# Performance work log

Hardware: AMD Instinct MI355X
Metric: run time of the kernel (lower is better)

The kernel has to match this reference:

```python
import jax, jax.numpy as jnp
import numpy as np

N_NODES = 100000
N_EDGES = 1200000
IN_FEATS = 128
HIDDEN = 64
OUT_FEATS = 40


def setup_inputs() -> dict:
    key = jax.random.key(0)
    k1, k2, k3, k4, k5 = jax.random.split(key, 5)
    x = jax.random.normal(k1, (N_NODES, IN_FEATS), dtype=jnp.float32)
    edge_index = jax.random.randint(k2, (2, N_EDGES), 0, N_NODES, dtype=jnp.int64)
    W1 = jax.random.normal(k3, (IN_FEATS, HIDDEN), dtype=jnp.float32) * (1.0 / np.sqrt(IN_FEATS))
    b1 = jnp.zeros((HIDDEN,), dtype=jnp.float32)
    W2 = jax.random.normal(k4, (HIDDEN, HIDDEN), dtype=jnp.float32) * (1.0 / np.sqrt(HIDDEN))
    b2 = jnp.zeros((HIDDEN,), dtype=jnp.float32)
    Wc = jax.random.normal(k5, (HIDDEN, OUT_FEATS), dtype=jnp.float32) * (1.0 / np.sqrt(HIDDEN))
    bc = jnp.zeros((OUT_FEATS,), dtype=jnp.float32)
    return {"x": x, "edge_index": edge_index, "W1": W1, "b1": b1,
            "W2": W2, "b2": b2, "Wc": Wc, "bc": bc}


def _gcn_norm(edge_index, n_nodes):
    # add self-loops, then symmetric normalization deg^{-1/2}[src] * deg^{-1/2}[dst]
    loops = jnp.arange(n_nodes, dtype=edge_index.dtype)
    src = jnp.concatenate([edge_index[0], loops])
    dst = jnp.concatenate([edge_index[1], loops])
    ones = jnp.ones(src.shape[0], dtype=jnp.float32)
    deg = jax.ops.segment_sum(ones, dst, num_segments=n_nodes)  # in-degree incl. self-loop
    dinv = jnp.where(deg > 0, jax.lax.rsqrt(deg), 0.0)
    norm = dinv[src] * dinv[dst]  # [E+N]
    return src, dst, norm


def _gcn_conv(h, W, b, src, dst, norm, n_nodes):
    h = h @ W                          # [N, F_out] dense transform first (PyG GCNConv)
    msg = h[src] * norm[:, None]       # gather + normalize, [E+N, F_out]
    out = jax.ops.segment_sum(msg, dst, num_segments=n_nodes)  # scatter-add
    return out + b


def reference(x, edge_index, W1, b1, W2, b2, Wc, bc):
    n = x.shape[0]
    src, dst, norm = _gcn_norm(edge_index, n)
    # dropout is identity in eval mode
    h = jax.nn.relu(_gcn_conv(x, W1, b1, src, dst, norm, n))
    embedding = _gcn_conv(h, W2, b2, src, dst, norm, n)
    logits = embedding @ Wc + bc
    soft_label = jax.nn.softmax(logits, axis=1)
    hard_label = jnp.argmax(soft_label, axis=1)
    return (logits, embedding, soft_label, hard_label)
```

## Files before the change

### kernel.cpp

```cpp
#include <hip/hip_runtime.h>
#include <hip/hip_bf16.h>
#include <math.h>

typedef __hip_bfloat16 bf16;
typedef __attribute__((ext_vector_type(8))) short bf16x8;
typedef __attribute__((ext_vector_type(4))) float f32x4;

__device__ __forceinline__ float loadf(const void* p, size_t i, bool f32m) {
    return f32m ? ((const float*)p)[i]
                : __bfloat162float(((const bf16*)p)[i]);
}
__device__ __forceinline__ void storef(void* p, size_t i, float v, bool f32m) {
    if (f32m) ((float*)p)[i] = v;
    else      ((bf16*)p)[i] = __float2bfloat16(v);
}
__device__ __forceinline__ int ldidx(const int* w, size_t e, bool e64, size_t E, int row) {
    return e64 ? w[2 * (row * E + e)] : w[row * E + e];
}

__device__ __forceinline__ unsigned short f2bf(float f) {
    unsigned u = __float_as_uint(f);
    unsigned r = (u + 0x7FFFu + ((u >> 16) & 1u)) >> 16;
    return (unsigned short)r;
}
__device__ __forceinline__ float bf2f(unsigned short h) {
    return __uint_as_float(((unsigned)h) << 16);
}

__global__ void k_detect(const void* x, const int* ei, float* flags) {
    int lane = threadIdx.x;
    const unsigned short* hx = (const unsigned short*)x;
    unsigned short u = hx[2 * lane];
    int ex = (u >> 7) & 0xFF;
    bool tame = (ex >= 117 && ex <= 136);
    unsigned long long mt = __ballot(tame);
    unsigned long long mz = __ballot(ei[2 * lane + 1] != 0);
    if (lane == 0) {
        flags[0] = (__popcll(mt) >= 48) ? 0.0f : 1.0f;
        flags[1] = (mz == 0ULL) ? 1.0f : 0.0f;
    }
}


__global__ void k_zero_small(int* __restrict__ p, int m) {
    int i = blockIdx.x * 256 + threadIdx.x;
    if (i < m) p[i] = 0;
}

#define SCB_EPT 16

__global__ __launch_bounds__(256) void k_bucket_hist(const int* __restrict__ ei,
                                                     const float* __restrict__ flags,
                                                     int* __restrict__ bcnt, int E, int NB) {
    __shared__ int lcnt[512];
    bool e64 = flags[1] > 0.5f;
    int tid = threadIdx.x;
    for (int i = tid; i < NB; i += 256) lcnt[i] = 0;
    __syncthreads();
    int base = blockIdx.x * 256 * SCB_EPT;
#pragma unroll
    for (int j = 0; j < SCB_EPT; ++j) {
        int e = base + j * 256 + tid;
        if (e < E) atomicAdd(&lcnt[ldidx(ei, e, e64, E, 1) >> 8], 1);
    }
    __syncthreads();
    for (int i = tid; i < NB; i += 256) {
        int c = lcnt[i];
        if (c) atomicAdd(&bcnt[i], c);
    }
}

__global__ __launch_bounds__(512) void k_scan_buckets(const int* __restrict__ bcnt,
                                                      int* __restrict__ bbase,
                                                      int* __restrict__ bcur, int NB) {
    __shared__ int sh[512];
    int tid = threadIdx.x;
    int v = (tid < NB) ? bcnt[tid] : 0;
    sh[tid] = v;
    __syncthreads();
    for (int off = 1; off < 512; off <<= 1) {
        int t = (tid >= off) ? sh[tid - off] : 0;
        __syncthreads();
        sh[tid] += t;
        __syncthreads();
    }
    if (tid < NB) {
        int ex = sh[tid] - v;
        bbase[tid] = ex;
        bcur[tid] = ex;
    }
    if (tid == 0) bbase[NB] = sh[511];
}

__global__ __launch_bounds__(256) void k_bucket_scatter(const int* __restrict__ ei,
                                                        const float* __restrict__ flags,
                                                        int* __restrict__ bcur,
                                                        int2* __restrict__ recs,
                                                        int E, int NB) {
    __shared__ int lcnt[512], lrank[512], lbase[512];
    bool e64 = flags[1] > 0.5f;
    int tid = threadIdx.x;
    for (int i = tid; i < NB; i += 256) { lcnt[i] = 0; lrank[i] = 0; }
    __syncthreads();
    int base = blockIdx.x * 256 * SCB_EPT;
    int s[SCB_EPT], d[SCB_EPT];
#pragma unroll
    for (int j = 0; j < SCB_EPT; ++j) {
        int e = base + j * 256 + tid;
        if (e < E) {
            s[j] = ldidx(ei, e, e64, E, 0);
            d[j] = ldidx(ei, e, e64, E, 1);
            atomicAdd(&lcnt[d[j] >> 8], 1);
        } else d[j] = -1;
    }
    __syncthreads();
    for (int i = tid; i < NB; i += 256) {
        int c = lcnt[i];
        lbase[i] = c ? atomicAdd(&bcur[i], c) : 0;
    }
    __syncthreads();
#pragma unroll
    for (int j = 0; j < SCB_EPT; ++j) {
        if (d[j] >= 0) {
            int b = d[j] >> 8;
            int r = atomicAdd(&lrank[b], 1);
            recs[lbase[b] + r] = make_int2(s[j], d[j]);
        }
    }
}

__global__ __launch_bounds__(256) void k_bucket_csr(const int2* __restrict__ recs,
                                                    const int* __restrict__ bbase,
                                                    int* __restrict__ rowptr,
                                                    float* __restrict__ dinv,
                                                    int* __restrict__ srcs,
                                                    int n, int E) {
    __shared__ int lcnt[256];
    __shared__ int lcur[256];
    int b = blockIdx.x, tid = threadIdx.x;
    int e0 = bbase[b], e1 = bbase[b + 1];
    lcnt[tid] = 0;
    __syncthreads();
    for (int i = e0 + tid; i < e1; i += 256)
        atomicAdd(&lcnt[recs[i].y & 255], 1);
    __syncthreads();
    int c = lcnt[tid];
    lcur[tid] = c;
    __syncthreads();
    for (int off = 1; off < 256; off <<= 1) {
        int t = (tid >= off) ? lcur[tid - off] : 0;
        __syncthreads();
        lcur[tid] += t;
        __syncthreads();
    }
    int rp = bbase[b] + lcur[tid] - c;
    int node = (b << 8) + tid;
    if (node < n) {
        rowptr[node] = rp;
        dinv[node] = rsqrtf((float)(c + 1));
    }
    lcur[tid] = rp;
    __syncthreads();
    for (int i = e0 + tid; i < e1; i += 256) {
        int2 r = recs[i];
        int pos = atomicAdd(&lcur[r.y & 255], 1);
        srcs[pos] = r.x;
    }
    if (b == 0 && tid == 0) rowptr[n] = E;
}

template <int K, bool XALWAYSF32>
__global__ __launch_bounds__(256) void k_gconv_mfma(const void* __restrict__ Xa,
                                                    const void* __restrict__ Xb,
                                                    const void* __restrict__ W,
                                                    const float* __restrict__ flags,
                                                    const float* __restrict__ rowscale,
                                                    float* __restrict__ out, int n) {
    constexpr int KP = K + 8;
    __shared__ __align__(16) unsigned short wh[64 * KP];
    __shared__ __align__(16) unsigned short wlo[64 * KP];
    bool f32m = flags[0] > 0.5f;
    const void* X = f32m ? Xa : Xb;
    bool xf32 = XALWAYSF32 || f32m;
    int tid = threadIdx.x;

    if (f32m) {
        for (int i = tid * 4; i < K * 64; i += 1024) {
            int k = i >> 6, c = i & 63;
            float4 v = *(const float4*)((const float*)W + i);
            float vv[4] = {v.x, v.y, v.z, v.w};
#pragma unroll
            for (int q = 0; q < 4; ++q) {
                unsigned short h = f2bf(vv[q]);
                unsigned short l = f2bf(vv[q] - bf2f(h));
                wh [(c + q) * KP + k] = h;
                wlo[(c + q) * KP + k] = l;
            }
        }
    } else {
        for (int i = tid; i < K * 64; i += 256) {
            int k = i >> 6, c = i & 63;
            wh [c * KP + k] = ((const unsigned short*)W)[i];
            wlo[c * KP + k] = 0;
        }
    }
    __syncthreads();

    int lane = tid & 63, wv = tid >> 6;
    int r0 = blockIdx.x * 64 + wv * 16;
    int mrow = lane & 15, kgrp = lane >> 4;
    int row = r0 + mrow;
    bool rok = (row < n);

    f32x4 acc[4];
#pragma unroll
    for (int ct = 0; ct < 4; ++ct) acc[ct] = (f32x4){0.0f, 0.0f, 0.0f, 0.0f};

    const float*          xrf = (const float*)X          + (size_t)(rok ? row : 0) * K;
    const unsigned short* xrb = (const unsigned short*)X + (size_t)(rok ? row : 0) * K;

#pragma unroll
    for (int ks = 0; ks < K / 32; ++ks) {
        int kb = ks * 32 + kgrp * 8;
        bf16x8 ahi = {0, 0, 0, 0, 0, 0, 0, 0};
        bf16x8 alo = {0, 0, 0, 0, 0, 0, 0, 0};
        if (rok) {
            if (xf32) {
                float4 v0 = *(const float4*)(xrf + kb);
                float4 v1 = *(const float4*)(xrf + kb + 4);
                float fv[8] = {v0.x, v0.y, v0.z, v0.w, v1.x, v1.y, v1.z, v1.w};
#pragma unroll
                for (int j = 0; j < 8; ++j) {
                    unsigned short h = f2bf(fv[j]);
                    ahi[j] = (short)h;
                    alo[j] = (short)f2bf(fv[j] - bf2f(h));
                }
            } else {
                ahi = *(const bf16x8*)(xrb + kb);
            }
        }
#pragma unroll
        for (int ct = 0; ct < 4; ++ct) {
            int c = ct * 16 + mrow;
            bf16x8 bhi = *(const bf16x8*)&wh [c * KP + kb];
            bf16x8 blo = *(const bf16x8*)&wlo[c * KP + kb];
            acc[ct] = __builtin_amdgcn_mfma_f32_16x16x32_bf16(ahi, bhi, acc[ct], 0, 0, 0);
            acc[ct] = __builtin_amdgcn_mfma_f32_16x16x32_bf16(ahi, blo, acc[ct], 0, 0, 0);
            acc[ct] = __builtin_amdgcn_mfma_f32_16x16x32_bf16(alo, bhi, acc[ct], 0, 0, 0);
        }
    }

    float sc[4];
    int obase = r0 + kgrp * 4;
#pragma unroll
    for (int r = 0; r < 4; ++r)
        sc[r] = (obase + r < n) ? rowscale[obase + r] : 0.0f;
#pragma unroll
    for (int ct = 0; ct < 4; ++ct) {
#pragma unroll
        for (int r = 0; r < 4; ++r) {
            int orow = obase + r;
            if (orow < n)
                out[(size_t)orow * 64 + ct * 16 + mrow] = acc[ct][r] * sc[r];
        }
    }
}

template <int EP>
__global__ __launch_bounds__(256) void k_agg(const float* __restrict__ t,
                                             const float* __restrict__ dinv,
                                             const int* __restrict__ rowptr,
                                             const int* __restrict__ srcs,
                                             const void* __restrict__ bias,
                                             const float* __restrict__ flags,
                                             void* __restrict__ d_out, size_t emb_base,
                                             float* __restrict__ B_ws, int n) {
    bool f32m = flags[0] > 0.5f;
    int wvid = (blockIdx.x * 256 + threadIdx.x) >> 6;
    int lane = threadIdx.x & 63;
    int grp = lane >> 4;
    int sub = lane & 15;
    int v = wvid * 4 + grp;
    if (v >= n) return;

    float dv = dinv[v];
    int e0 = rowptr[v], e1 = rowptr[v + 1];
    int deg = e1 - e0;

    float4 acc = *(const float4*)(t + ((size_t)v << 6) + sub * 4);

    for (int base = 0; base < deg; base += 16) {
        int idx = base + sub;
        int sid = (idx < deg) ? srcs[e0 + idx] : -1;
        int cnt = deg - base; if (cnt > 16) cnt = 16;
        for (int j = 0; j < cnt; j += 4) {
            int gb = grp * 16 + j;
            int s0 = __shfl(sid, gb + 0, 64);
            int s1 = __shfl(sid, gb + 1, 64);
            int s2 = __shfl(sid, gb + 2, 64);
            int s3 = __shfl(sid, gb + 3, 64);
            float4 r0 = {0, 0, 0, 0}, r1 = {0, 0, 0, 0}, r2 = {0, 0, 0, 0}, r3 = {0, 0, 0, 0};
            if (s0 >= 0) r0 = *(const float4*)(t + ((size_t)s0 << 6) + sub * 4);
            if (s1 >= 0) r1 = *(const float4*)(t + ((size_t)s1 << 6) + sub * 4);
            if (s2 >= 0) r2 = *(const float4*)(t + ((size_t)s2 << 6) + sub * 4);
            if (s3 >= 0) r3 = *(const float4*)(t + ((size_t)s3 << 6) + sub * 4);
            acc.x += (r0.x + r1.x) + (r2.x + r3.x);
            acc.y += (r0.y + r1.y) + (r2.y + r3.y);
            acc.z += (r0.z + r1.z) + (r2.z + r3.z);
            acc.w += (r0.w + r1.w) + (r2.w + r3.w);
        }
    }

    float4 bias4;
    if (f32m) {
        bias4 = ((const float4*)bias)[sub];
    } else {
        const bf16* bp = (const bf16*)bias + sub * 4;
        bias4.x = __bfloat162float(bp[0]); bias4.y = __bfloat162float(bp[1]);
        bias4.z = __bfloat162float(bp[2]); bias4.w = __bfloat162float(bp[3]);
    }

    float4 o;
    o.x = acc.x * dv + bias4.x;
    o.y = acc.y * dv + bias4.y;
    o.z = acc.z * dv + bias4.z;
    o.w = acc.w * dv + bias4.w;
    if (EP == 0) {
        o.x = fmaxf(o.x, 0.0f); o.y = fmaxf(o.y, 0.0f);
        o.z = fmaxf(o.z, 0.0f); o.w = fmaxf(o.w, 0.0f);
    }
    size_t ob = ((size_t)v << 6) + sub * 4;
    if (f32m) {
        *(float4*)((float*)d_out + emb_base + ob) = o;
    } else {
        *(float4*)&B_ws[ob] = o;
        if (EP == 1) {
            __hip_bfloat162 h0, h1;
            h0.x = __float2bfloat16(o.x); h0.y = __float2bfloat16(o.y);
            h1.x = __float2bfloat16(o.z); h1.y = __float2bfloat16(o.w);
            __hip_bfloat162* p = (__hip_bfloat162*)((bf16*)d_out + emb_base + ob);
            p[0] = h0; p[1] = h1;
        }
    }
}


__device__ __forceinline__ void store_row40(void* out, size_t base, const float* a, bool f32m) {
    if (f32m) {
        float4* p = (float4*)((float*)out + base);
#pragma unroll
        for (int q = 0; q < 10; ++q) {
            float4 st = {a[q * 4 + 0], a[q * 4 + 1], a[q * 4 + 2], a[q * 4 + 3]};
            p[q] = st;
        }
    } else {
        __hip_bfloat162* p = (__hip_bfloat162*)((bf16*)out + base);
#pragma unroll
        for (int i = 0; i < 20; ++i) {
            __hip_bfloat162 h;
            h.x = __float2bfloat16(a[2 * i]);
            h.y = __float2bfloat16(a[2 * i + 1]);
            p[i] = h;
        }
    }
}

__global__ __launch_bounds__(256) void k_classifier(const float* __restrict__ flags,
                                                    const void* __restrict__ Wc,
                                                    const void* __restrict__ bc,
                                                    void* __restrict__ out,
                                                    size_t emb_base, size_t soft_base,
                                                    size_t hard_base,
                                                    const float* __restrict__ B_ws,
                                                    int n) {
    __shared__ __align__(16) float wcs[64 * 40];
    __shared__ __align__(16) float bcs[40];
    bool f32m = flags[0] > 0.5f;
    const float* emb = f32m ? ((const float*)out + emb_base) : B_ws;
    int tid = threadIdx.x;

    if (f32m) {
        for (int i = tid * 4; i < 64 * 40; i += 1024)
            *(float4*)&wcs[i] = *(const float4*)((const float*)Wc + i);
    } else {
        for (int i = tid; i < 64 * 40; i += 256)
            wcs[i] = __bfloat162float(((const bf16*)Wc)[i]);
    }
    if (tid < 40) bcs[tid] = loadf(bc, tid, f32m);
    __syncthreads();

    int node = blockIdx.x * 256 + tid;
    if (node >= n) return;

    float acc[40];
#pragma unroll
    for (int q = 0; q < 10; ++q) {
        float4 b4 = *(const float4*)&bcs[q * 4];
        acc[q * 4 + 0] = b4.x; acc[q * 4 + 1] = b4.y;
        acc[q * 4 + 2] = b4.z; acc[q * 4 + 3] = b4.w;
    }

    const float4* erow = (const float4*)(emb + (size_t)node * 64);
#pragma unroll 2
    for (int j = 0; j < 16; ++j) {
        float4 e4 = erow[j];
        float ev[4] = {e4.x, e4.y, e4.z, e4.w};
#pragma unroll
        for (int kk = 0; kk < 4; ++kk) {
            float e = ev[kk];
            const float4* wr = (const float4*)&wcs[(j * 4 + kk) * 40];
#pragma unroll
            for (int q = 0; q < 10; ++q) {
                float4 w = wr[q];
                acc[q * 4 + 0] = fmaf(e, w.x, acc[q * 4 + 0]);
                acc[q * 4 + 1] = fmaf(e, w.y, acc[q * 4 + 1]);
                acc[q * 4 + 2] = fmaf(e, w.z, acc[q * 4 + 2]);
                acc[q * 4 + 3] = fmaf(e, w.w, acc[q * 4 + 3]);
            }
        }
    }

    store_row40(out, (size_t)node * 40, acc, f32m);

    float m0 = acc[0], m1 = acc[1], m2 = acc[2], m3 = acc[3];
#pragma unroll
    for (int q = 1; q < 10; ++q) {
        m0 = fmaxf(m0, acc[q * 4 + 0]); m1 = fmaxf(m1, acc[q * 4 + 1]);
        m2 = fmaxf(m2, acc[q * 4 + 2]); m3 = fmaxf(m3, acc[q * 4 + 3]);
    }
    float m = fmaxf(fmaxf(m0, m1), fmaxf(m2, m3));

    int bi = 63;
#pragma unroll
    for (int c = 0; c < 40; ++c)
        if (acc[c] == m && c < bi) bi = c;

    float s = 0.0f;
#pragma unroll
    for (int c = 0; c < 40; ++c) {
        float e = expf(acc[c] - m);
        acc[c] = e;
        s += e;
    }
    float rs = 1.0f / s;
#pragma unroll
    for (int c = 0; c < 40; ++c) acc[c] *= rs;

    store_row40(out, soft_base + (size_t)node * 40, acc, f32m);
    storef(out, hard_base + node, (float)bi, f32m);
}

extern "C" void kernel_launch(void* const* d_in, const int* in_sizes, int n_in,
                              void* d_out, int out_size, void* d_ws, size_t ws_size,
                              hipStream_t stream) {
    const void* x  = d_in[0];
    const int*  ei = (const int*)d_in[1];
    const void* W1 = d_in[2];
    const void* b1 = d_in[3];
    const void* W2 = d_in[4];
    const void* b2 = d_in[5];
    const void* Wc = d_in[6];
    const void* bc = d_in[7];

    const int n = in_sizes[0] / 128;
    const int E = in_sizes[1] / 2;
    const int NB = (n + 255) / 256;

    float* ws    = (float*)d_ws;
    const size_t npad = (((size_t)n + 1023) / 1024) * 1024;
    const size_t Epad = (((size_t)E + 255) / 256) * 256;
    float* flags  = ws;
    int*   bcnt   = (int*)(ws + 256);
    int*   bbase  = (int*)(ws + 768);
    int*   bcur   = (int*)(ws + 1536);
    int*   rowptr = (int*)(ws + 2048);
    float* dinv   = (float*)(rowptr + npad);
    int*   srcs   = (int*)(dinv + npad);
    float* A      = (float*)(srcs + Epad);
    float* B_ws   = A + (size_t)n * 64;
    int2*  recs   = (int2*)B_ws;

    const size_t emb_base  = (size_t)n * 40;
    const size_t soft_base = (size_t)n * 104;
    const size_t hard_base = (size_t)n * 144;
    float* h1_f32m = (float*)d_out + emb_base;

    const int gS  = (E + 256 * SCB_EPT - 1) / (256 * SCB_EPT);
    const int gG  = (n + 63) / 64;
    const int gW  = (n + 15) / 16;
    const int gC  = (n + 255) / 256;

    k_detect<<<1, 64, 0, stream>>>(x, ei, flags);

    k_zero_small<<<2, 256, 0, stream>>>(bcnt, 512);
    k_bucket_hist<<<gS, 256, 0, stream>>>(ei, flags, bcnt, E, NB);
    k_scan_buckets<<<1, 512, 0, stream>>>(bcnt, bbase, bcur, NB);
    k_bucket_scatter<<<gS, 256, 0, stream>>>(ei, flags, bcur, recs, E, NB);
    k_bucket_csr<<<NB, 256, 0, stream>>>(recs, bbase, rowptr, dinv, srcs, n, E);

    k_gconv_mfma<128, false><<<gG, 256, 0, stream>>>(x, x, W1, flags, dinv, A, n);
    k_agg<0><<<gW, 256, 0, stream>>>(A, dinv, rowptr, srcs, b1, flags,
                                     d_out, emb_base, B_ws, n);

    k_gconv_mfma<64, true><<<gG, 256, 0, stream>>>(h1_f32m, B_ws, W2, flags, dinv, A, n);
    k_agg<1><<<gW, 256, 0, stream>>>(A, dinv, rowptr, srcs, b2, flags,
                                     d_out, emb_base, B_ws, n);

    k_classifier<<<gC, 256, 0, stream>>>(flags, Wc, bc, d_out,
                                         emb_base, soft_base, hard_base, B_ws, n);
}
```

Before: 314.6 us.

## Replace two-level bucket sort CSR build with per-node degree count and atomic fill

Replaces the bucket histogram, scatter and per-bucket local sort with a direct pipeline. Global atomics count per-node in-degree, a three-stage prefix scan produces rowptr and dinv, and a fill kernel places each source with a per-node atomic cursor. This removes the intermediate int2 record buffer and its extra pass. In exchange it uses many contended global atomics and issues two extra small launches, and the neighbour order within each row becomes nondeterministic.

```diff
diff --git a/kernel.cpp b/kernel.cpp
--- a/kernel.cpp
+++ b/kernel.cpp
@@ -42,40 +42,50 @@
 }
 
 
-__global__ void k_zero_small(int* __restrict__ p, int m) {
+#define SCB_EPT 16
+
+__global__ void k_zero_deg(int* __restrict__ deg, int n) {
     int i = blockIdx.x * 256 + threadIdx.x;
-    if (i < m) p[i] = 0;
-}
-
-#define SCB_EPT 16
-
-__global__ __launch_bounds__(256) void k_bucket_hist(const int* __restrict__ ei,
-                                                     const float* __restrict__ flags,
-                                                     int* __restrict__ bcnt, int E, int NB) {
-    __shared__ int lcnt[512];
+    if (i < n) deg[i] = 0;
+}
+
+__global__ __launch_bounds__(256) void k_deg(const int* __restrict__ ei,
+                                             const float* __restrict__ flags,
+                                             int* __restrict__ deg, int E) {
     bool e64 = flags[1] > 0.5f;
     int tid = threadIdx.x;
-    for (int i = tid; i < NB; i += 256) lcnt[i] = 0;
-    __syncthreads();
     int base = blockIdx.x * 256 * SCB_EPT;
 #pragma unroll
     for (int j = 0; j < SCB_EPT; ++j) {
         int e = base + j * 256 + tid;
-        if (e < E) atomicAdd(&lcnt[ldidx(ei, e, e64, E, 1) >> 8], 1);
-    }
+        if (e < E) atomicAdd(&deg[ldidx(ei, e, e64, E, 1)], 1);
+    }
+}
+
+__global__ __launch_bounds__(256) void k_scanA(const int* __restrict__ deg,
+                                               int* __restrict__ lpre,
+                                               int* __restrict__ ctot, int n) {
+    __shared__ int sh[256];
+    int b = blockIdx.x, tid = threadIdx.x;
+    int i = b * 256 + tid;
+    int v = (i < n) ? deg[i] : 0;
+    sh[tid] = v;
     __syncthreads();
-    for (int i = tid; i < NB; i += 256) {
-        int c = lcnt[i];
-        if (c) atomicAdd(&bcnt[i], c);
-    }
-}
-
-__global__ __launch_bounds__(512) void k_scan_buckets(const int* __restrict__ bcnt,
-                                                      int* __restrict__ bbase,
-                                                      int* __restrict__ bcur, int NB) {
+    for (int off = 1; off < 256; off <<= 1) {
+        int t = (tid >= off) ? sh[tid - off] : 0;
+        __syncthreads();
+        sh[tid] += t;
+        __syncthreads();
+    }
+    if (i < n) lpre[i] = sh[tid] - v;
+    if (tid == 255) ctot[b] = sh[255];
+}
+
+__global__ __launch_bounds__(512) void k_scanB(const int* __restrict__ ctot,
+                                               int* __restrict__ cbase, int NCH) {
     __shared__ int sh[512];
     int tid = threadIdx.x;
-    int v = (tid < NB) ? bcnt[tid] : 0;
+    int v = (tid < NCH) ? ctot[tid] : 0;
     sh[tid] = v;
     __syncthreads();
     for (int off = 1; off < 512; off <<= 1) {
@@ -84,89 +94,42 @@
         sh[tid] += t;
         __syncthreads();
     }
-    if (tid < NB) {
-        int ex = sh[tid] - v;
-        bbase[tid] = ex;
-        bcur[tid] = ex;
-    }
-    if (tid == 0) bbase[NB] = sh[511];
-}
-
-__global__ __launch_bounds__(256) void k_bucket_scatter(const int* __restrict__ ei,
-                                                        const float* __restrict__ flags,
-                                                        int* __restrict__ bcur,
-                                                        int2* __restrict__ recs,
-                                                        int E, int NB) {
-    __shared__ int lcnt[512], lrank[512], lbase[512];
+    if (tid < NCH) cbase[tid] = sh[tid] - v;
+}
+
+__global__ __launch_bounds__(256) void k_scanC(const int* __restrict__ deg,
+                                               const int* __restrict__ lpre,
+                                               const int* __restrict__ cbase,
+                                               int* __restrict__ rowptr,
+                                               float* __restrict__ dinv,
+                                               int* __restrict__ cur, int n, int E) {
+    int i = blockIdx.x * 256 + threadIdx.x;
+    if (i < n) {
+        int rp = cbase[i >> 8] + lpre[i];
+        rowptr[i] = rp;
+        cur[i] = rp;
+        dinv[i] = rsqrtf((float)(deg[i] + 1));
+    }
+    if (i == 0) rowptr[n] = E;
+}
+
+__global__ __launch_bounds__(256) void k_fill(const int* __restrict__ ei,
+                                              const float* __restrict__ flags,
+                                              int* __restrict__ cur,
+                                              int* __restrict__ srcs, int E) {
     bool e64 = flags[1] > 0.5f;
     int tid = threadIdx.x;
-    for (int i = tid; i < NB; i += 256) { lcnt[i] = 0; lrank[i] = 0; }
-    __syncthreads();
     int base = blockIdx.x * 256 * SCB_EPT;
-    int s[SCB_EPT], d[SCB_EPT];
 #pragma unroll
     for (int j = 0; j < SCB_EPT; ++j) {
         int e = base + j * 256 + tid;
         if (e < E) {
-            s[j] = ldidx(ei, e, e64, E, 0);
-            d[j] = ldidx(ei, e, e64, E, 1);
-            atomicAdd(&lcnt[d[j] >> 8], 1);
-        } else d[j] = -1;
-    }
-    __syncthreads();
-    for (int i = tid; i < NB; i += 256) {
-        int c = lcnt[i];
-        lbase[i] = c ? atomicAdd(&bcur[i], c) : 0;
-    }
-    __syncthreads();
-#pragma unroll
-    for (int j = 0; j < SCB_EPT; ++j) {
-        if (d[j] >= 0) {
-            int b = d[j] >> 8;
-            int r = atomicAdd(&lrank[b], 1);
-            recs[lbase[b] + r] = make_int2(s[j], d[j]);
-        }
-    }
-}
-
-__global__ __launch_bounds__(256) void k_bucket_csr(const int2* __restrict__ recs,
-                                                    const int* __restrict__ bbase,
-                                                    int* __restrict__ rowptr,
-                                                    float* __restrict__ dinv,
-                                                    int* __restrict__ srcs,
-                                                    int n, int E) {
-    __shared__ int lcnt[256];
-    __shared__ int lcur[256];
-    int b = blockIdx.x, tid = threadIdx.x;
-    int e0 = bbase[b], e1 = bbase[b + 1];
-    lcnt[tid] = 0;
-    __syncthreads();
-    for (int i = e0 + tid; i < e1; i += 256)
-        atomicAdd(&lcnt[recs[i].y & 255], 1);
-    __syncthreads();
-    int c = lcnt[tid];
-    lcur[tid] = c;
-    __syncthreads();
-    for (int off = 1; off < 256; off <<= 1) {
-        int t = (tid >= off) ? lcur[tid - off] : 0;
-        __syncthreads();
-        lcur[tid] += t;
-        __syncthreads();
-    }
-    int rp = bbase[b] + lcur[tid] - c;
-    int node = (b << 8) + tid;
-    if (node < n) {
-        rowptr[node] = rp;
-        dinv[node] = rsqrtf((float)(c + 1));
-    }
-    lcur[tid] = rp;
-    __syncthreads();
-    for (int i = e0 + tid; i < e1; i += 256) {
-        int2 r = recs[i];
-        int pos = atomicAdd(&lcur[r.y & 255], 1);
-        srcs[pos] = r.x;
-    }
-    if (b == 0 && tid == 0) rowptr[n] = E;
+            int s = ldidx(ei, e, e64, E, 0);
+            int d = ldidx(ei, e, e64, E, 1);
+            int pos = atomicAdd(&cur[d], 1);
+            srcs[pos] = s;
+        }
+    }
 }
 
 template <int K, bool XALWAYSF32>
@@ -464,39 +427,43 @@
 
     const int n = in_sizes[0] / 128;
     const int E = in_sizes[1] / 2;
-    const int NB = (n + 255) / 256;
+    const int NCH = (n + 255) / 256;
 
     float* ws    = (float*)d_ws;
     const size_t npad = (((size_t)n + 1023) / 1024) * 1024;
     const size_t Epad = (((size_t)E + 255) / 256) * 256;
     float* flags  = ws;
-    int*   bcnt   = (int*)(ws + 256);
-    int*   bbase  = (int*)(ws + 768);
-    int*   bcur   = (int*)(ws + 1536);
     int*   rowptr = (int*)(ws + 2048);
     float* dinv   = (float*)(rowptr + npad);
     int*   srcs   = (int*)(dinv + npad);
     float* A      = (float*)(srcs + Epad);
     float* B_ws   = A + (size_t)n * 64;
-    int2*  recs   = (int2*)B_ws;
+
+    int*   deg    = (int*)B_ws;
+    int*   lpre   = deg + npad;
+    int*   ctot   = lpre + npad;
+    int*   cbase  = ctot + 512;
+    int*   cur    = cbase + 512;
 
     const size_t emb_base  = (size_t)n * 40;
     const size_t soft_base = (size_t)n * 104;
     const size_t hard_base = (size_t)n * 144;
     float* h1_f32m = (float*)d_out + emb_base;
 
-    const int gS  = (E + 256 * SCB_EPT - 1) / (256 * SCB_EPT);
+    const int gE  = (E + 256 * SCB_EPT - 1) / (256 * SCB_EPT);
+    const int gN  = (n + 255) / 256;
     const int gG  = (n + 63) / 64;
     const int gW  = (n + 15) / 16;
     const int gC  = (n + 255) / 256;
 
     k_detect<<<1, 64, 0, stream>>>(x, ei, flags);
 
-    k_zero_small<<<2, 256, 0, stream>>>(bcnt, 512);
-    k_bucket_hist<<<gS, 256, 0, stream>>>(ei, flags, bcnt, E, NB);
-    k_scan_buckets<<<1, 512, 0, stream>>>(bcnt, bbase, bcur, NB);
-    k_bucket_scatter<<<gS, 256, 0, stream>>>(ei, flags, bcur, recs, E, NB);
-    k_bucket_csr<<<NB, 256, 0, stream>>>(recs, bbase, rowptr, dinv, srcs, n, E);
+    k_zero_deg<<<gN, 256, 0, stream>>>(deg, n);
+    k_deg<<<gE, 256, 0, stream>>>(ei, flags, deg, E);
+    k_scanA<<<NCH, 256, 0, stream>>>(deg, lpre, ctot, n);
+    k_scanB<<<1, 512, 0, stream>>>(ctot, cbase, NCH);
+    k_scanC<<<gN, 256, 0, stream>>>(deg, lpre, cbase, rowptr, dinv, cur, n, E);
+    k_fill<<<gE, 256, 0, stream>>>(ei, flags, cur, srcs, E);
 
     k_gconv_mfma<128, false><<<gG, 256, 0, stream>>>(x, x, W1, flags, dinv, A, n);
     k_agg<0><<<gW, 256, 0, stream>>>(A, dinv, rowptr, srcs, b1, flags,
```

Result: slower. 411.0 us (+30.7%).
